# Optimization experiments

Measured on AMD Instinct MI355X. Metric: run time of the kernel, lower is better.

The kernel has to match this reference:

```python
import jax, jax.numpy as jnp
import numpy as np

D_MODEL = 1024
NUM_HEADS = 16
D_K = D_MODEL // NUM_HEADS
D_FF = 4096
LN_EPS = 1e-5


def layer_norm(x, gamma, beta):
    mu = jnp.mean(x, axis=-1, keepdims=True)
    var = jnp.var(x, axis=-1, keepdims=True)
    return (x - mu) * jax.lax.rsqrt(var + LN_EPS) * gamma + beta


def setup_inputs() -> dict:
    key = jax.random.key(0)
    ks = jax.random.split(key, 10)
    s = 0.02
    return {
        "x": jax.random.normal(ks[0], (2, 2048, D_MODEL), dtype=jnp.float32),
        # per-head projections stacked: [H, d_model, d_k] (equivalent to the
        # num_heads separate nn.Linear(d_model, d_k, bias=False) modules)
        "Wq": jax.random.normal(ks[1], (NUM_HEADS, D_MODEL, D_K), dtype=jnp.float32) * s,
        "Wk": jax.random.normal(ks[2], (NUM_HEADS, D_MODEL, D_K), dtype=jnp.float32) * s,
        "Wv": jax.random.normal(ks[3], (NUM_HEADS, D_MODEL, D_K), dtype=jnp.float32) * s,
        "Wo": jax.random.normal(ks[4], (D_MODEL, D_MODEL), dtype=jnp.float32) * s,
        "W1": jax.random.normal(ks[5], (D_MODEL, D_FF), dtype=jnp.float32) * s,
        "b1": jnp.zeros((D_FF,), dtype=jnp.float32),
        "W2": jax.random.normal(ks[6], (D_FF, D_MODEL), dtype=jnp.float32) * s,
        "b2": jnp.zeros((D_MODEL,), dtype=jnp.float32),
        "g1": jnp.ones((D_MODEL,), dtype=jnp.float32),
        "beta1": jnp.zeros((D_MODEL,), dtype=jnp.float32),
        "g2": jnp.ones((D_MODEL,), dtype=jnp.float32),
        "beta2": jnp.zeros((D_MODEL,), dtype=jnp.float32),
    }


def reference(x, Wq, Wk, Wv, Wo, W1, b1, W2, b2, g1, beta1, g2, beta2):
    B, S, D = x.shape
    # ---- pre-LN multi-head self-attention ----
    h = layer_norm(x, g1, beta1)
    # batched QKV projections (equivalent to the per-head Python loop)
    Q = jnp.einsum('bsd,hdk->bhsk', h, Wq)  # [B,H,S,dk]
    K = jnp.einsum('bsd,hdk->bhsk', h, Wk)
    V = jnp.einsum('bsd,hdk->bhsk', h, Wv)
    scores = jnp.einsum('bhqk,bhsk->bhqs', Q, K) / jnp.sqrt(jnp.asarray(D_K, x.dtype))
    weights = jax.nn.softmax(scores, axis=-1)  # [B,H,S,S]
    attn = jnp.einsum('bhqs,bhsk->bhqk', weights, V)  # [B,H,S,dk]
    # concat heads along feature dim (head order preserved)
    concat = attn.transpose(0, 2, 1, 3).reshape(B, S, D)
    x = x + concat @ Wo
    # ---- pre-LN FFN (exact erf GELU, matching nn.GELU default) ----
    h2 = layer_norm(x, g2, beta2)
    ffn = jax.nn.gelu(h2 @ W1 + b1, approximate=False) @ W2 + b2
    return x + ffn
```

## Files before the change

### kernel.cpp

```cpp
#include <hip/hip_runtime.h>
#include <stdint.h>


typedef __attribute__((ext_vector_type(8))) short bf16x8;
typedef __attribute__((ext_vector_type(4))) float f32x4;
typedef __attribute__((ext_vector_type(16))) float f32x16;
typedef __attribute__((ext_vector_type(4))) unsigned short u16x4;
typedef __attribute__((ext_vector_type(4))) unsigned int u32x4;

#define DEV __device__ __forceinline__

static constexpr int DM   = 1024;
static constexpr int DFF  = 4096;
static constexpr int NH   = 16;
static constexpr int DKH  = 64;
static constexpr int SEQ  = 2048;
static constexpr int NBAT = 2;
static constexpr int NTOK = NBAT * SEQ;

DEV unsigned short f2bf(float f) {
  union { float f; unsigned int u; } v; v.f = f;
  unsigned int u = v.u;
  return (unsigned short)((u + 0x7fffu + ((u >> 16) & 1u)) >> 16);
}

DEV void gload_lds16(const unsigned short* g, unsigned short* l) {
  __builtin_amdgcn_global_load_lds(
      (const __attribute__((address_space(1))) unsigned int*)g,
      (__attribute__((address_space(3))) unsigned int*)l, 16, 0, 0);
}

DEV float fast_gelu(float x) {
  const float z = fabsf(x) * 0.70710678118654752f;
  const float t = __builtin_amdgcn_rcpf(1.0f + 0.3275911f * z);
  float p = 1.061405429f;
  p = p * t - 1.453152027f;
  p = p * t + 1.421413741f;
  p = p * t - 0.284496736f;
  p = p * t + 0.254829592f;
  p = p * t;
  float erfv = 1.0f - p * __expf(-z * z);
  erfv = copysignf(erfv, x);
  return 0.5f * x * (1.0f + erfv);
}

__global__ __launch_bounds__(256) void ln_kernel(
    const float* __restrict__ x, const float* __restrict__ g,
    const float* __restrict__ be, unsigned short* __restrict__ out) {
  const int row = blockIdx.x;
  const int t = threadIdx.x;
  const int lane = t & 63, w = t >> 6;
  const float4* xr = (const float4*)(x + (size_t)row * DM);
  float4 v = xr[t];
  float s  = v.x + v.y + v.z + v.w;
  float s2 = v.x * v.x + v.y * v.y + v.z * v.z + v.w * v.w;
#pragma unroll
  for (int off = 32; off; off >>= 1) {
    s  += __shfl_down(s, off);
    s2 += __shfl_down(s2, off);
  }
  __shared__ float rs_[4], rq_[4];
  if (lane == 0) { rs_[w] = s; rq_[w] = s2; }
  __syncthreads();
  float fs = rs_[0] + rs_[1] + rs_[2] + rs_[3];
  float fq = rq_[0] + rq_[1] + rq_[2] + rq_[3];
  float mu = fs * (1.0f / DM);
  float var = fq * (1.0f / DM) - mu * mu;
  float rstd = rsqrtf(var + 1e-5f);
  float4 gv = ((const float4*)g)[t];
  float4 bv = ((const float4*)be)[t];
  u16x4 o;
  o[0] = f2bf((v.x - mu) * rstd * gv.x + bv.x);
  o[1] = f2bf((v.y - mu) * rstd * gv.y + bv.y);
  o[2] = f2bf((v.z - mu) * rstd * gv.z + bv.z);
  o[3] = f2bf((v.w - mu) * rstd * gv.w + bv.w);
  *(u16x4*)(out + (size_t)row * DM + t * 4) = o;
}

__global__ __launch_bounds__(256) void transpose_weights(
    const float* __restrict__ Wq, const float* __restrict__ Wk,
    const float* __restrict__ Wv, const float* __restrict__ Wo,
    const float* __restrict__ W1, const float* __restrict__ W2,
    unsigned short* __restrict__ wqkv_t, unsigned short* __restrict__ wo_t,
    unsigned short* __restrict__ w1_t, unsigned short* __restrict__ w2_t) {
  __shared__ float lds[64][65];
  const int t = blockIdx.x;
  const float* inb; unsigned short* outb; int in_ld, out_ld;
  if (t < 768) {
    const int slice = t >> 4, tin = t & 15;
    const int which = slice >> 4, h = slice & 15;
    const float* W = (which == 0) ? Wq : (which == 1) ? Wk : Wv;
    inb = W + (size_t)((h << 10) + (tin << 6)) * 64;
    in_ld = 64;
    outb = wqkv_t + ((size_t)((which << 10) + (h << 6)) << 10) + (tin << 6);
    out_ld = 1024;
  } else if (t < 1024) {
    const int tt = t - 768, tr = tt >> 4, tc = tt & 15;
    inb = Wo + (size_t)(tc << 6) * 1024 + (tr << 6); in_ld = 1024;
    outb = wo_t + (size_t)(tr << 6) * 1024 + (tc << 6); out_ld = 1024;
  } else if (t < 2048) {
    const int tt = t - 1024, tr = tt >> 4, tc = tt & 15;
    inb = W1 + (size_t)(tc << 6) * 4096 + (tr << 6); in_ld = 4096;
    outb = w1_t + (size_t)(tr << 6) * 1024 + (tc << 6); out_ld = 1024;
  } else {
    const int tt = t - 2048, tr = tt >> 6, tc = tt & 63;
    inb = W2 + (size_t)(tc << 6) * 1024 + (tr << 6); in_ld = 1024;
    outb = w2_t + (size_t)(tr << 6) * 4096 + (tc << 6); out_ld = 4096;
  }
  const int j = threadIdx.x & 63, i0 = threadIdx.x >> 6;
#pragma unroll
  for (int p = 0; p < 16; ++p) {
    const int i = i0 + p * 4;
    lds[j][i] = inb[(size_t)i * in_ld + j];
  }
  __syncthreads();
#pragma unroll
  for (int p = 0; p < 16; ++p) {
    const int r = i0 + p * 4;
    outb[(size_t)r * out_ld + j] = f2bf(lds[r][j]);
  }
}

struct EpiArgs {
  unsigned short* q;
  unsigned short* k;
  unsigned short* vt;
  unsigned short* ob16;
  float* of32;
  float* p0;
  const float* bias;
  const float* resid;
};

template <int EPI>
DEV void epilogue_elem(float v, int row, int col, int N, int bz,
                       const EpiArgs& ep) {
  if constexpr (EPI == 0) {
    const int bb = row >> 11, rr = row & 2047;
    if (col < 1024) {
      const int hh = col >> 6, dk = col & 63;
      const int kk = dk >> 4, h8 = (dk >> 3) & 1, e = dk & 7;
      const int qblk = rr >> 5, l31 = rr & 31;
      ep.q[((size_t)(bb * NH + hh) * 64 + qblk) * 2048 + kk * 512 +
           (h8 * 32 + l31) * 8 + e] = f2bf(v * 0.18033688011112042f);
    } else if (col < 2048) {
      const int c = col - 1024;
      const int hh = c >> 6, dk = c & 63;
      const int kk = dk >> 4, h8 = (dk >> 3) & 1, e = dk & 7;
      const int kvblk = rr >> 5, l31 = rr & 31;
      ep.k[((size_t)(bb * NH + hh) * 64 + kvblk) * 2048 + kk * 512 +
           (h8 * 32 + l31) * 8 + e] = f2bf(v);
    } else {
      const int c = col - 2048, hh = c >> 6, dd = c & 63;
      const int ssw = (rr & ~12) | ((rr & 4) << 1) | ((rr & 8) >> 1);
      const int t64 = ssw >> 6, w = (ssw >> 4) & 3;
      const int h8 = (ssw >> 3) & 1, e = ssw & 7;
      const int dblk = dd >> 5, l31 = dd & 31;
      ep.vt[(((size_t)(bb * NH + hh) * 32 + t64) * 8 + dblk * 4 + w) * 512 +
            (h8 * 32 + l31) * 8 + e] = f2bf(v);
    }
  } else if constexpr (EPI == 1) {
    const size_t idx = (size_t)row * N + col;
    ep.of32[idx] = v + ep.resid[idx];
  } else if constexpr (EPI == 2) {
    ep.ob16[(size_t)row * N + col] = f2bf(fast_gelu(v + ep.bias[col]));
  } else {
    const size_t idx = (size_t)row * N + col;
    if (bz == 0) ep.p0[idx] = v;
    else ep.of32[idx] = ep.of32[idx] + v + ep.bias[col];
  }
}

template <int EPI>
__global__ __launch_bounds__(512, 2) void gemm_256(
    const unsigned short* __restrict__ A, const unsigned short* __restrict__ Bt,
    int N, int K, int ldk, EpiArgs ep) {
  __shared__ __align__(16) unsigned short Als[2][256 * 64];
  __shared__ __align__(16) unsigned short Bls[2][256 * 64];
  const int t = threadIdx.x, lane = t & 63, wave = t >> 6;
  const int wm = wave >> 2, wn = wave & 3;
  const int g = lane >> 4, r16 = lane & 15;
  const int nx = gridDim.x, nwg = nx * gridDim.y;
  int wgid = blockIdx.y * nx + blockIdx.x;
  wgid = (wgid & 7) * (nwg >> 3) + (wgid >> 3);
  const int m0 = (wgid / nx) * 256, n0 = (wgid % nx) * 256;

  f32x4 acc[8][4];
  const f32x4 z4 = {0.f, 0.f, 0.f, 0.f};
#pragma unroll
  for (int i = 0; i < 8; ++i)
#pragma unroll
    for (int j = 0; j < 4; ++j) acc[i][j] = z4;

  auto stage_half = [&](int b, int k0, int h) {
#pragma unroll
    for (int i = 0; i < 2; ++i) {
      const int c = i * 512 + t;
      const int row = c >> 3;
      const int sc = ((c & 7) ^ (row & 7)) * 8;
      const int dofs = ((h & 1) << 13) + (i * 512 + (wave << 6)) * 8;
      if (h < 2)
        gload_lds16(A + (size_t)(m0 + ((h & 1) << 7) + row) * ldk + k0 + sc,
                    &Als[b][dofs]);
      else
        gload_lds16(Bt + (size_t)(n0 + ((h & 1) << 7) + row) * ldk + k0 + sc,
                    &Bls[b][dofs]);
    }
  };

  const int NT = K >> 6;
#pragma unroll
  for (int h = 0; h < 4; ++h) stage_half(0, 0, h);

  for (int kt = 0; kt < NT; ++kt) {
    const int cur = kt & 1;
    const bool more = (kt + 1) < NT;
    const int nk0 = (kt + 1) << 6;
    __builtin_amdgcn_s_barrier();
    if (more) {
      stage_half(cur ^ 1, nk0, 0);
      stage_half(cur ^ 1, nk0, 1);
      asm volatile("s_waitcnt vmcnt(4)" ::: "memory");
    } else {
      asm volatile("s_waitcnt vmcnt(0)" ::: "memory");
    }
    __builtin_amdgcn_s_barrier();
    __builtin_amdgcn_sched_barrier(0);

    bf16x8 Af[8][2];
#pragma unroll
    for (int mf = 0; mf < 8; ++mf) {
      const int row = (wm << 7) + (mf << 4) + r16;
#pragma unroll
      for (int ks = 0; ks < 2; ++ks)
        Af[mf][ks] = *(const bf16x8*)
            &Als[cur][row * 64 + ((((ks << 2) | g) ^ (row & 7)) << 3)];
    }
#pragma unroll
    for (int qn = 0; qn < 2; ++qn) {
      bf16x8 Bf[2][2];
#pragma unroll
      for (int ni = 0; ni < 2; ++ni) {
        const int row = (wn << 6) + (((qn << 1) | ni) << 4) + r16;
#pragma unroll
        for (int ks = 0; ks < 2; ++ks)
          Bf[ni][ks] = *(const bf16x8*)
              &Bls[cur][row * 64 + ((((ks << 2) | g) ^ (row & 7)) << 3)];
      }
      __builtin_amdgcn_s_setprio(1);
#pragma unroll
      for (int ks = 0; ks < 2; ++ks)
#pragma unroll
        for (int mf = 0; mf < 8; ++mf)
#pragma unroll
          for (int ni = 0; ni < 2; ++ni)
            acc[mf][(qn << 1) | ni] = __builtin_amdgcn_mfma_f32_16x16x32_bf16(
                Af[mf][ks], Bf[ni][ks], acc[mf][(qn << 1) | ni], 0, 0, 0);
      __builtin_amdgcn_s_setprio(0);
      if (qn == 0 && more) {
        stage_half(cur ^ 1, nk0, 2);
        stage_half(cur ^ 1, nk0, 3);
      }
    }
  }
#pragma unroll
  for (int mf = 0; mf < 8; ++mf)
#pragma unroll
    for (int nf = 0; nf < 4; ++nf)
#pragma unroll
      for (int r = 0; r < 4; ++r)
        epilogue_elem<EPI>(acc[mf][nf][r],
                           m0 + (wm << 7) + (mf << 4) + (g << 2) + r,
                           n0 + (wn << 6) + (nf << 4) + r16, N, 0, ep);
}

template <int EPI>
__global__ __launch_bounds__(256) void gemm_pipe(
    const unsigned short* __restrict__ A, const unsigned short* __restrict__ Bt,
    int N, int Kc, int ldk, EpiArgs ep) {
  __shared__ __align__(16) unsigned short Als[2][128 * 64];
  __shared__ __align__(16) unsigned short Bls[2][128 * 64];
  const int t = threadIdx.x, lane = t & 63, wave = t >> 6;
  const int wm = wave >> 1, wn = wave & 1;
  const int g = lane >> 4, r16 = lane & 15;
  const int nx = gridDim.x;
  const int nwg = nx * gridDim.y;
  int wgid = blockIdx.y * nx + blockIdx.x;
  wgid = (wgid & 7) * (nwg >> 3) + (wgid >> 3);
  const int m0 = (wgid / nx) * 128, n0 = (wgid % nx) * 128;
  const int kbase = blockIdx.z * Kc;

  f32x4 acc[4][4];
  const f32x4 z4 = {0.f, 0.f, 0.f, 0.f};
#pragma unroll
  for (int i = 0; i < 4; ++i)
#pragma unroll
    for (int j = 0; j < 4; ++j) acc[i][j] = z4;

  auto stage = [&](int b, int k0) {
#pragma unroll
    for (int i = 0; i < 4; ++i) {
      const int cb = i * 256 + wave * 64;
      const int c = cb + lane;
      const int row = c >> 3;
      const int sc = ((c & 7) ^ (row & 7)) * 8;
      gload_lds16(A + (size_t)(m0 + row) * ldk + kbase + k0 + sc, &Als[b][cb * 8]);
      gload_lds16(Bt + (size_t)(n0 + row) * ldk + kbase + k0 + sc, &Bls[b][cb * 8]);
    }
  };

  const int NT = Kc >> 6;
  stage(0, 0);
  __syncthreads();
  for (int kt = 0; kt < NT; ++kt) {
    const int cur = kt & 1;
    if (kt + 1 < NT) stage(cur ^ 1, (kt + 1) << 6);
    const int sw = r16 & 7;
    bf16x8 af[2][4], bfr[2][4];
#pragma unroll
    for (int ks = 0; ks < 2; ++ks) {
#pragma unroll
      for (int mt = 0; mt < 4; ++mt)
        af[ks][mt] = *(const bf16x8*)&Als[cur][(wm * 64 + mt * 16 + r16) * 64 +
                                              (((ks << 2) | g) ^ sw) * 8];
#pragma unroll
      for (int nt = 0; nt < 4; ++nt)
        bfr[ks][nt] = *(const bf16x8*)&Bls[cur][(wn * 64 + nt * 16 + r16) * 64 +
                                               (((ks << 2) | g) ^ sw) * 8];
    }
    __builtin_amdgcn_s_setprio(1);
#pragma unroll
    for (int ks = 0; ks < 2; ++ks)
#pragma unroll
      for (int mt = 0; mt < 4; ++mt)
#pragma unroll
        for (int nt = 0; nt < 4; ++nt)
          acc[mt][nt] = __builtin_amdgcn_mfma_f32_16x16x32_bf16(
              af[ks][mt], bfr[ks][nt], acc[mt][nt], 0, 0, 0);
    __builtin_amdgcn_s_setprio(0);
    __syncthreads();
  }
#pragma unroll
  for (int mt = 0; mt < 4; ++mt)
#pragma unroll
    for (int nt = 0; nt < 4; ++nt)
#pragma unroll
      for (int r = 0; r < 4; ++r)
        epilogue_elem<EPI>(acc[mt][nt][r], m0 + wm * 64 + mt * 16 + g * 4 + r,
                           n0 + wn * 64 + nt * 16 + r16, N, blockIdx.z, ep);
}

__global__ __launch_bounds__(256) void reduce_add(const float* __restrict__ p,
                                                  float* __restrict__ out) {
  const int i = blockIdx.x * 256 + threadIdx.x;
  float4 a = ((const float4*)p)[i];
  float4 b = ((float4*)out)[i];
  b.x += a.x; b.y += a.y; b.z += a.z; b.w += a.w;
  ((float4*)out)[i] = b;
}

struct AttnState {
  f32x16 o0, o1;
  float m, lsum;
};

DEV void load_k(const unsigned short* kbase, int s, bf16x8 k0[4], bf16x8 k1[4]) {
  const unsigned short* p = kbase + (size_t)(s >> 5) * 2048;
#pragma unroll
  for (int kk = 0; kk < 4; ++kk) {
    k0[kk] = *(const bf16x8*)(p + kk * 512);
    k1[kk] = *(const bf16x8*)(p + 2048 + kk * 512);
  }
}

DEV void attn_tile(const bf16x8 k0[4], const bf16x8 k1[4],
                   const bf16x8 v0[4], const bf16x8 v1[4],
                   const bf16x8 qf[4], AttnState& st) {
  const f32x16 z16 = {0.f};
  f32x16 pA = z16, pB = z16;
  __builtin_amdgcn_s_setprio(1);
#pragma unroll
  for (int kk = 0; kk < 4; ++kk) {
    pA = __builtin_amdgcn_mfma_f32_32x32x16_bf16(k0[kk], qf[kk], pA, 0, 0, 0);
    pB = __builtin_amdgcn_mfma_f32_32x32x16_bf16(k1[kk], qf[kk], pB, 0, 0, 0);
  }
  __builtin_amdgcn_s_setprio(0);
  float m0 = fmaxf(pA[0], pB[0]), m1 = fmaxf(pA[1], pB[1]);
  float m2 = fmaxf(pA[2], pB[2]), m3 = fmaxf(pA[3], pB[3]);
#pragma unroll
  for (int r = 4; r < 16; r += 4) {
    m0 = fmaxf(m0, fmaxf(pA[r + 0], pB[r + 0]));
    m1 = fmaxf(m1, fmaxf(pA[r + 1], pB[r + 1]));
    m2 = fmaxf(m2, fmaxf(pA[r + 2], pB[r + 2]));
    m3 = fmaxf(m3, fmaxf(pA[r + 3], pB[r + 3]));
  }
  float mx = fmaxf(fmaxf(m0, m1), fmaxf(m2, m3));
  mx = fmaxf(mx, __shfl_xor(mx, 32));
  if (__any(mx > st.m + 11.5416f)) {
    const float mnew = fmaxf(st.m, mx);
    const float corr = __builtin_amdgcn_exp2f(st.m - mnew);
#pragma unroll
    for (int r = 0; r < 16; ++r) { st.o0[r] *= corr; st.o1[r] *= corr; }
    st.lsum *= corr;
    st.m = mnew;
  }
  float ps = 0.f;
#pragma unroll
  for (int r = 0; r < 16; ++r) {
    pA[r] = __builtin_amdgcn_exp2f(pA[r] - st.m); ps += pA[r];
    pB[r] = __builtin_amdgcn_exp2f(pB[r] - st.m); ps += pB[r];
  }
  ps += __shfl_xor(ps, 32);
  st.lsum += ps;
  bf16x8 pw[4];
#pragma unroll
  for (int w = 0; w < 4; ++w) {
    unsigned int wd0, wd1, wd2, wd3;
    const int e0 = (w & 1) * 8;
    if (w < 2) {
      asm("v_cvt_pk_bf16_f32 %0, %1, %2" : "=v"(wd0) : "v"(pA[e0 + 0]), "v"(pA[e0 + 1]));
      asm("v_cvt_pk_bf16_f32 %0, %1, %2" : "=v"(wd1) : "v"(pA[e0 + 2]), "v"(pA[e0 + 3]));
      asm("v_cvt_pk_bf16_f32 %0, %1, %2" : "=v"(wd2) : "v"(pA[e0 + 4]), "v"(pA[e0 + 5]));
      asm("v_cvt_pk_bf16_f32 %0, %1, %2" : "=v"(wd3) : "v"(pA[e0 + 6]), "v"(pA[e0 + 7]));
    } else {
      asm("v_cvt_pk_bf16_f32 %0, %1, %2" : "=v"(wd0) : "v"(pB[e0 + 0]), "v"(pB[e0 + 1]));
      asm("v_cvt_pk_bf16_f32 %0, %1, %2" : "=v"(wd1) : "v"(pB[e0 + 2]), "v"(pB[e0 + 3]));
      asm("v_cvt_pk_bf16_f32 %0, %1, %2" : "=v"(wd2) : "v"(pB[e0 + 4]), "v"(pB[e0 + 5]));
      asm("v_cvt_pk_bf16_f32 %0, %1, %2" : "=v"(wd3) : "v"(pB[e0 + 6]), "v"(pB[e0 + 7]));
    }
    u32x4 wv = {wd0, wd1, wd2, wd3};
    pw[w] = __builtin_bit_cast(bf16x8, wv);
  }
  __builtin_amdgcn_s_setprio(1);
#pragma unroll
  for (int w = 0; w < 4; ++w) {
    st.o0 = __builtin_amdgcn_mfma_f32_32x32x16_bf16(v0[w], pw[w], st.o0, 0, 0, 0);
    st.o1 = __builtin_amdgcn_mfma_f32_32x32x16_bf16(v1[w], pw[w], st.o1, 0, 0, 0);
  }
  __builtin_amdgcn_s_setprio(0);
}

__global__ __launch_bounds__(256, 2) void attn_kernel(
    const unsigned short* __restrict__ Qc, const unsigned short* __restrict__ Kc,
    const unsigned short* __restrict__ Vt, unsigned short* __restrict__ Oc) {
  const int lane = threadIdx.x & 63, wave = threadIdx.x >> 6;
  const int hi = lane >> 5, l31 = lane & 31;
  const int i = blockIdx.x;
  const int k8 = i & 7, mq = i >> 3;
  const int grp = k8 + 8 * (mq >> 4);
  const int qb = mq & 15;
  const int b = grp >> 4, h = grp & 15;
  const int q0 = qb * 128 + wave * 32;

  const unsigned short* qbp = Qc + ((size_t)grp * 64 + (q0 >> 5)) * 2048 + lane * 8;
  const unsigned short* kbp = Kc + (size_t)grp * 64 * 2048 + lane * 8;
  const unsigned short* vbp = Vt + (size_t)grp * 32 * 4096 + lane * 8;

  bf16x8 qf[4];
#pragma unroll
  for (int kk = 0; kk < 4; ++kk) qf[kk] = *(const bf16x8*)(qbp + kk * 512);

  AttnState st;
#pragma unroll
  for (int r = 0; r < 16; ++r) { st.o0[r] = 0.f; st.o1[r] = 0.f; }
  st.m = -1e30f; st.lsum = 0.f;

  bf16x8 kA0[4], kA1[4], kB0[4], kB1[4];
  load_k(kbp, 0, kA0, kA1);

  for (int s0 = 0; s0 < SEQ; s0 += 128) {
    const unsigned short* vt0 = vbp + (size_t)(s0 >> 6) * 4096;
    bf16x8 v0[4], v1[4];
#pragma unroll
    for (int w = 0; w < 4; ++w) {
      v0[w] = *(const bf16x8*)(vt0 + w * 512);
      v1[w] = *(const bf16x8*)(vt0 + 2048 + w * 512);
    }
    load_k(kbp, s0 + 64, kB0, kB1);
    attn_tile(kA0, kA1, v0, v1, qf, st);
    const unsigned short* vt1 = vbp + (size_t)((s0 + 64) >> 6) * 4096;
#pragma unroll
    for (int w = 0; w < 4; ++w) {
      v0[w] = *(const bf16x8*)(vt1 + w * 512);
      v1[w] = *(const bf16x8*)(vt1 + 2048 + w * 512);
    }
    const int snext = (s0 + 128 < SEQ) ? (s0 + 128) : 0;
    load_k(kbp, snext, kA0, kA1);
    attn_tile(kB0, kB1, v0, v1, qf, st);
  }

  const float inv = 1.0f / st.lsum;
  const size_t rowbase = (size_t)b * SEQ;
  unsigned short* op = Oc + (rowbase + q0 + l31) * DM + h * DKH + hi * 4;
#pragma unroll
  for (int dblk = 0; dblk < 2; ++dblk)
#pragma unroll
    for (int g4 = 0; g4 < 4; ++g4) {
      u16x4 stv;
#pragma unroll
      for (int r = 0; r < 4; ++r) {
        const float v = (dblk ? st.o1[g4 * 4 + r] : st.o0[g4 * 4 + r]) * inv;
        stv[r] = f2bf(v);
      }
      *(u16x4*)(op + dblk * 32 + g4 * 8) = stv;
    }
}

extern "C" void kernel_launch(void* const* d_in, const int* in_sizes, int n_in,
                              void* d_out, int out_size, void* d_ws,
                              size_t ws_size, hipStream_t stream) {
  (void)in_sizes; (void)n_in; (void)out_size; (void)ws_size;
  const float* x   = (const float*)d_in[0];
  const float* Wq  = (const float*)d_in[1];
  const float* Wk  = (const float*)d_in[2];
  const float* Wv  = (const float*)d_in[3];
  const float* Wo  = (const float*)d_in[4];
  const float* W1  = (const float*)d_in[5];
  const float* b1  = (const float*)d_in[6];
  const float* W2  = (const float*)d_in[7];
  const float* b2  = (const float*)d_in[8];
  const float* g1  = (const float*)d_in[9];
  const float* be1 = (const float*)d_in[10];
  const float* g2  = (const float*)d_in[11];
  const float* be2 = (const float*)d_in[12];
  float* out = (float*)d_out;

  char* ws = (char*)d_ws;
  const size_t MB = 1024 * 1024;
  unsigned short* h_buf  = (unsigned short*)(ws + 0 * MB);
  unsigned short* wqkv_t = (unsigned short*)(ws + 8 * MB);
  unsigned short* wo_t   = (unsigned short*)(ws + 14 * MB);
  unsigned short* w1_t   = (unsigned short*)(ws + 16 * MB);
  unsigned short* w2_t   = (unsigned short*)(ws + 24 * MB);
  unsigned short* q_attn = (unsigned short*)(ws + 32 * MB);
  unsigned short* k_attn = (unsigned short*)(ws + 40 * MB);
  unsigned short* v_attn = (unsigned short*)(ws + 48 * MB);
  unsigned short* ffn1   = (unsigned short*)(ws + 32 * MB);
  float*          p0     = (float*)(ws + 0 * MB);

  EpiArgs e0 = {}; e0.q = q_attn; e0.k = k_attn; e0.vt = v_attn;
  EpiArgs e1 = {}; e1.of32 = out; e1.resid = x;
  EpiArgs e2 = {}; e2.ob16 = ffn1; e2.bias = b1;
  EpiArgs e4 = {}; e4.of32 = out; e4.p0 = p0; e4.bias = b2;

  transpose_weights<<<3072, 256, 0, stream>>>(Wq, Wk, Wv, Wo, W1, W2,
                                              wqkv_t, wo_t, w1_t, w2_t);
  ln_kernel<<<NTOK, 256, 0, stream>>>(x, g1, be1, h_buf);
  gemm_256<0><<<dim3(3072 / 256, NTOK / 256), 512, 0, stream>>>(
      h_buf, wqkv_t, 3072, DM, DM, e0);
  attn_kernel<<<512, 256, 0, stream>>>(q_attn, k_attn, v_attn, h_buf);
  gemm_pipe<1><<<dim3(DM / 128, NTOK / 128, 1), 256, 0, stream>>>(
      h_buf, wo_t, DM, DM, DM, e1);
  ln_kernel<<<NTOK, 256, 0, stream>>>(out, g2, be2, h_buf);
  gemm_256<2><<<dim3(DFF / 256, NTOK / 256), 512, 0, stream>>>(
      h_buf, w1_t, DFF, DM, DM, e2);
  gemm_pipe<4><<<dim3(DM / 128, NTOK / 128, 2), 256, 0, stream>>>(
      ffn1, w2_t, DM, DFF / 2, DFF, e4);
  reduce_add<<<4096, 256, 0, stream>>>(p0, out);
}
```

Before: 254.7 us.

## Software-pipeline attention: overlap next tile's QK^T MFMA with current softmax/PV

Splits the attention tile into a QK^T stage and a softmax+PV stage, then software-pipelines the loop so the next tile's score MFMAs are issued before the current tile's softmax and PV. The goal is to hide exp and reduction latency behind matrix-core work and to cut the K register buffers from two sets to one. It also splits the softmax row-sum into four independent accumulators to shorten the dependency chain. In exchange it keeps two sets of 32x32 score accumulators live, which raises VGPR pressure and may reduce occupancy.

```diff
diff --git a/kernel.cpp b/kernel.cpp
--- a/kernel.cpp
+++ b/kernel.cpp
@@ -373,11 +373,19 @@
   }
 }
 
-DEV void attn_tile(const bf16x8 k0[4], const bf16x8 k1[4],
-                   const bf16x8 v0[4], const bf16x8 v1[4],
-                   const bf16x8 qf[4], AttnState& st) {
+DEV void load_v(const unsigned short* vbp, int s, bf16x8 v0[4], bf16x8 v1[4]) {
+  const unsigned short* vt = vbp + (size_t)(s >> 6) * 4096;
+#pragma unroll
+  for (int w = 0; w < 4; ++w) {
+    v0[w] = *(const bf16x8*)(vt + w * 512);
+    v1[w] = *(const bf16x8*)(vt + 2048 + w * 512);
+  }
+}
+
+DEV void attn_qk(const bf16x8 k0[4], const bf16x8 k1[4], const bf16x8 qf[4],
+                 f32x16& pA, f32x16& pB) {
   const f32x16 z16 = {0.f};
-  f32x16 pA = z16, pB = z16;
+  pA = z16; pB = z16;
   __builtin_amdgcn_s_setprio(1);
 #pragma unroll
   for (int kk = 0; kk < 4; ++kk) {
@@ -385,6 +393,10 @@
     pB = __builtin_amdgcn_mfma_f32_32x32x16_bf16(k1[kk], qf[kk], pB, 0, 0, 0);
   }
   __builtin_amdgcn_s_setprio(0);
+}
+
+DEV void attn_smpv(f32x16& pA, f32x16& pB, const bf16x8 v0[4],
+                   const bf16x8 v1[4], AttnState& st) {
   float m0 = fmaxf(pA[0], pB[0]), m1 = fmaxf(pA[1], pB[1]);
   float m2 = fmaxf(pA[2], pB[2]), m3 = fmaxf(pA[3], pB[3]);
 #pragma unroll
@@ -404,12 +416,19 @@
     st.lsum *= corr;
     st.m = mnew;
   }
-  float ps = 0.f;
-#pragma unroll
-  for (int r = 0; r < 16; ++r) {
-    pA[r] = __builtin_amdgcn_exp2f(pA[r] - st.m); ps += pA[r];
-    pB[r] = __builtin_amdgcn_exp2f(pB[r] - st.m); ps += pB[r];
-  }
+  float ps0 = 0.f, ps1 = 0.f, ps2 = 0.f, ps3 = 0.f;
+#pragma unroll
+  for (int r = 0; r < 16; r += 4) {
+    pA[r + 0] = __builtin_amdgcn_exp2f(pA[r + 0] - st.m); ps0 += pA[r + 0];
+    pA[r + 1] = __builtin_amdgcn_exp2f(pA[r + 1] - st.m); ps1 += pA[r + 1];
+    pA[r + 2] = __builtin_amdgcn_exp2f(pA[r + 2] - st.m); ps2 += pA[r + 2];
+    pA[r + 3] = __builtin_amdgcn_exp2f(pA[r + 3] - st.m); ps3 += pA[r + 3];
+    pB[r + 0] = __builtin_amdgcn_exp2f(pB[r + 0] - st.m); ps0 += pB[r + 0];
+    pB[r + 1] = __builtin_amdgcn_exp2f(pB[r + 1] - st.m); ps1 += pB[r + 1];
+    pB[r + 2] = __builtin_amdgcn_exp2f(pB[r + 2] - st.m); ps2 += pB[r + 2];
+    pB[r + 3] = __builtin_amdgcn_exp2f(pB[r + 3] - st.m); ps3 += pB[r + 3];
+  }
+  float ps = (ps0 + ps1) + (ps2 + ps3);
   ps += __shfl_xor(ps, 32);
   st.lsum += ps;
   bf16x8 pw[4];
@@ -465,28 +484,24 @@
   for (int r = 0; r < 16; ++r) { st.o0[r] = 0.f; st.o1[r] = 0.f; }
   st.m = -1e30f; st.lsum = 0.f;
 
-  bf16x8 kA0[4], kA1[4], kB0[4], kB1[4];
-  load_k(kbp, 0, kA0, kA1);
-
+  bf16x8 kf0[4], kf1[4];
+  f32x16 P0A, P0B, P1A, P1B;
+  load_k(kbp, 0, kf0, kf1);
+  attn_qk(kf0, kf1, qf, P0A, P0B);
+  load_k(kbp, 64, kf0, kf1);
+
+  bf16x8 v0[4], v1[4];
   for (int s0 = 0; s0 < SEQ; s0 += 128) {
-    const unsigned short* vt0 = vbp + (size_t)(s0 >> 6) * 4096;
-    bf16x8 v0[4], v1[4];
-#pragma unroll
-    for (int w = 0; w < 4; ++w) {
-      v0[w] = *(const bf16x8*)(vt0 + w * 512);
-      v1[w] = *(const bf16x8*)(vt0 + 2048 + w * 512);
-    }
-    load_k(kbp, s0 + 64, kB0, kB1);
-    attn_tile(kA0, kA1, v0, v1, qf, st);
-    const unsigned short* vt1 = vbp + (size_t)((s0 + 64) >> 6) * 4096;
-#pragma unroll
-    for (int w = 0; w < 4; ++w) {
-      v0[w] = *(const bf16x8*)(vt1 + w * 512);
-      v1[w] = *(const bf16x8*)(vt1 + 2048 + w * 512);
-    }
-    const int snext = (s0 + 128 < SEQ) ? (s0 + 128) : 0;
-    load_k(kbp, snext, kA0, kA1);
-    attn_tile(kB0, kB1, v0, v1, qf, st);
+    load_v(vbp, s0, v0, v1);
+    attn_qk(kf0, kf1, qf, P1A, P1B);
+    int sn = s0 + 128; if (sn >= SEQ) sn = 0;
+    load_k(kbp, sn, kf0, kf1);
+    attn_smpv(P0A, P0B, v0, v1, st);
+    load_v(vbp, s0 + 64, v0, v1);
+    attn_qk(kf0, kf1, qf, P0A, P0B);
+    int sn2 = s0 + 192; if (sn2 >= SEQ) sn2 = 64;
+    load_k(kbp, sn2, kf0, kf1);
+    attn_smpv(P1A, P1B, v0, v1, st);
   }
 
   const float inv = 1.0f / st.lsum;
```

After: 257.7 us. No clear change (+1.2%).

## Split attention over key halves and merge partial outputs in a separate kernel

Applied to the files above, without the earlier changes.

The attention kernel now splits each query block's key/value range into two halves, doubling the grid from 512 to 1024 blocks. Each block writes an unnormalized bf16 partial output plus its running max and sum. A new merge kernel combines the two halves with log-sum-exp rescaling and normalizes the result into the buffer that the output projection reads. Launch bounds are raised to allow 4 blocks per CU. The aim is to fill the GPU better, in the style of split-KV flash decoding. The cost is an extra kernel launch, extra memory traffic for the partials, possible register pressure or spills under the tighter launch bound, and an extra bf16 rounding of the unnormalized partials.

```diff
diff --git a/kernel.cpp b/kernel.cpp
--- a/kernel.cpp
+++ b/kernel.cpp
@@ -22,6 +22,11 @@
   union { float f; unsigned int u; } v; v.f = f;
   unsigned int u = v.u;
   return (unsigned short)((u + 0x7fffu + ((u >> 16) & 1u)) >> 16);
+}
+
+DEV float bf2f(unsigned short s) {
+  union { unsigned int u; float f; } v; v.u = ((unsigned int)s) << 16;
+  return v.f;
 }
 
 DEV void gload_lds16(const unsigned short* g, unsigned short* l) {
@@ -440,15 +445,17 @@
   __builtin_amdgcn_s_setprio(0);
 }
 
-__global__ __launch_bounds__(256, 2) void attn_kernel(
+__global__ __launch_bounds__(256, 4) void attn_kernel(
     const unsigned short* __restrict__ Qc, const unsigned short* __restrict__ Kc,
-    const unsigned short* __restrict__ Vt, unsigned short* __restrict__ Oc) {
+    const unsigned short* __restrict__ Vt, unsigned short* __restrict__ pO0,
+    unsigned short* __restrict__ pO1, float2* __restrict__ ml) {
   const int lane = threadIdx.x & 63, wave = threadIdx.x >> 6;
   const int hi = lane >> 5, l31 = lane & 31;
   const int i = blockIdx.x;
   const int k8 = i & 7, mq = i >> 3;
-  const int grp = k8 + 8 * (mq >> 4);
-  const int qb = mq & 15;
+  const int grp = k8 + 8 * (mq >> 5);
+  const int inner = mq & 31;
+  const int qb = inner & 15, half = inner >> 4;
   const int b = grp >> 4, h = grp & 15;
   const int q0 = qb * 128 + wave * 32;
 
@@ -465,10 +472,11 @@
   for (int r = 0; r < 16; ++r) { st.o0[r] = 0.f; st.o1[r] = 0.f; }
   st.m = -1e30f; st.lsum = 0.f;
 
+  const int sbase = half << 10;
   bf16x8 kA0[4], kA1[4], kB0[4], kB1[4];
-  load_k(kbp, 0, kA0, kA1);
-
-  for (int s0 = 0; s0 < SEQ; s0 += 128) {
+  load_k(kbp, sbase, kA0, kA1);
+
+  for (int s0 = sbase; s0 < sbase + 1024; s0 += 128) {
     const unsigned short* vt0 = vbp + (size_t)(s0 >> 6) * 4096;
     bf16x8 v0[4], v1[4];
 #pragma unroll
@@ -484,26 +492,57 @@
       v0[w] = *(const bf16x8*)(vt1 + w * 512);
       v1[w] = *(const bf16x8*)(vt1 + 2048 + w * 512);
     }
-    const int snext = (s0 + 128 < SEQ) ? (s0 + 128) : 0;
+    const int snext = (s0 + 128 < sbase + 1024) ? (s0 + 128) : sbase;
     load_k(kbp, snext, kA0, kA1);
     attn_tile(kB0, kB1, v0, v1, qf, st);
   }
 
-  const float inv = 1.0f / st.lsum;
+  unsigned short* pO = half ? pO1 : pO0;
   const size_t rowbase = (size_t)b * SEQ;
-  unsigned short* op = Oc + (rowbase + q0 + l31) * DM + h * DKH + hi * 4;
+  unsigned short* op = pO + (rowbase + q0 + l31) * DM + h * DKH + hi * 4;
 #pragma unroll
   for (int dblk = 0; dblk < 2; ++dblk)
 #pragma unroll
     for (int g4 = 0; g4 < 4; ++g4) {
       u16x4 stv;
 #pragma unroll
-      for (int r = 0; r < 4; ++r) {
-        const float v = (dblk ? st.o1[g4 * 4 + r] : st.o0[g4 * 4 + r]) * inv;
-        stv[r] = f2bf(v);
-      }
+      for (int r = 0; r < 4; ++r)
+        stv[r] = f2bf(dblk ? st.o1[g4 * 4 + r] : st.o0[g4 * 4 + r]);
       *(u16x4*)(op + dblk * 32 + g4 * 8) = stv;
     }
+  if (hi == 0) {
+    float2 v; v.x = st.m; v.y = st.lsum;
+    ml[(size_t)((half * 32 + grp) << 11) + q0 + l31] = v;
+  }
+}
+
+__global__ __launch_bounds__(256) void merge_attn(
+    const unsigned short* __restrict__ p0, const unsigned short* __restrict__ p1,
+    const float2* __restrict__ ml, unsigned short* __restrict__ out) {
+  const int tid = blockIdx.x * 256 + threadIdx.x;
+  const int row = tid >> 7;
+  const int c8 = (tid & 127) << 3;
+  const int b = row >> 11, s = row & 2047;
+  const int h = c8 >> 6;
+  const int grp = b * NH + h;
+  const float2 A = ml[(size_t)(grp << 11) + s];
+  const float2 Bv = ml[(size_t)((32 + grp) << 11) + s];
+  const float mm = fmaxf(A.x, Bv.x);
+  const float ca = __builtin_amdgcn_exp2f(A.x - mm);
+  const float cb = __builtin_amdgcn_exp2f(Bv.x - mm);
+  const float inv = 1.0f / (A.y * ca + Bv.y * cb);
+  const float fa = ca * inv, fb = cb * inv;
+  const size_t base = (size_t)row * DM + c8;
+  u16x4 a0 = *(const u16x4*)(p0 + base), a1 = *(const u16x4*)(p0 + base + 4);
+  u16x4 b0 = *(const u16x4*)(p1 + base), b1 = *(const u16x4*)(p1 + base + 4);
+  u16x4 o0, o1;
+#pragma unroll
+  for (int r = 0; r < 4; ++r) {
+    o0[r] = f2bf(bf2f(a0[r]) * fa + bf2f(b0[r]) * fb);
+    o1[r] = f2bf(bf2f(a1[r]) * fa + bf2f(b1[r]) * fb);
+  }
+  *(u16x4*)(out + base) = o0;
+  *(u16x4*)(out + base + 4) = o1;
 }
 
 extern "C" void kernel_launch(void* const* d_in, const int* in_sizes, int n_in,
@@ -536,6 +575,8 @@
   unsigned short* k_attn = (unsigned short*)(ws + 40 * MB);
   unsigned short* v_attn = (unsigned short*)(ws + 48 * MB);
   unsigned short* ffn1   = (unsigned short*)(ws + 32 * MB);
+  unsigned short* pO1    = (unsigned short*)(ws + 56 * MB);
+  float2*         mlbuf  = (float2*)(ws + 8 * MB);
   float*          p0     = (float*)(ws + 0 * MB);
 
   EpiArgs e0 = {}; e0.q = q_attn; e0.k = k_attn; e0.vt = v_attn;
@@ -548,7 +589,9 @@
   ln_kernel<<<NTOK, 256, 0, stream>>>(x, g1, be1, h_buf);
   gemm_256<0><<<dim3(3072 / 256, NTOK / 256), 512, 0, stream>>>(
       h_buf, wqkv_t, 3072, DM, DM, e0);
-  attn_kernel<<<512, 256, 0, stream>>>(q_attn, k_attn, v_attn, h_buf);
+  attn_kernel<<<1024, 256, 0, stream>>>(q_attn, k_attn, v_attn,
+                                        h_buf, pO1, mlbuf);
+  merge_attn<<<4096, 256, 0, stream>>>(h_buf, pO1, mlbuf, h_buf);
   gemm_pipe<1><<<dim3(DM / 128, NTOK / 128, 1), 256, 0, stream>>>(
       h_buf, wo_t, DM, DM, DM, e1);
   ln_kernel<<<NTOK, 256, 0, stream>>>(out, g2, be2, h_buf);
```

Result: slower. 394.7 us (+55.0%).
